# Kernel tuning notes

Measured on AMD Instinct MI355X. Metric: run time of the kernel, lower is better.

The kernel has to match this reference:

```python
import jax, jax.numpy as jnp
import numpy as np

NUM_FEATURES = 256
NUM_PIDS = 5554          # must equal hardcoded FocalLoss ignore_index
NUM_CQ = 50000
N_ROIS = 2048
OIM_SCALAR = 30.0
IGNORE_INDEX = 5554
ALPHA = 1.0
GAMMA = 2.0


def _l2norm(x):
    return x / jnp.linalg.norm(x, axis=-1, keepdims=True)


def setup_inputs() -> dict:
    key = jax.random.key(0)
    k1, k2, k3, k4, k5 = jax.random.split(key, 5)
    inputs = _l2norm(jax.random.normal(k1, (N_ROIS, NUM_FEATURES), jnp.float32))
    # targets >= 1 so label = targets-1 >= 0 (the inds filter is all-True -> static shapes)
    # targets == NUM_PIDS+1 -> label == NUM_PIDS == ignore_index (unlabeled, ignored in loss)
    targets = jax.random.randint(k2, (N_ROIS,), 1, NUM_PIDS + 2, dtype=jnp.int64)
    ious = jax.random.uniform(k3, (N_ROIS,), jnp.float32)
    lut = _l2norm(jax.random.normal(k4, (NUM_PIDS, NUM_FEATURES), jnp.float32))
    cq = _l2norm(jax.random.normal(k5, (NUM_CQ, NUM_FEATURES), jnp.float32))
    return {"inputs": inputs, "lut": lut, "cq": cq, "targets": targets, "ious": ious}


def _focal_loss(logits, labels):
    # F.cross_entropy(reduction='none', ignore_index=IGNORE_INDEX) then
    # focal = alpha * (1-pt)^gamma * ce, mean over ALL samples (ignored -> 0).
    logp = jax.nn.log_softmax(logits, axis=-1)                       # [N, C]
    ce = -jnp.take_along_axis(logp, labels[:, None], axis=1)[:, 0]   # [N]
    ce = jnp.where(labels == IGNORE_INDEX, 0.0, ce)
    pt = jnp.exp(-ce)
    return jnp.mean(ALPHA * (1.0 - pt) ** GAMMA * ce)


def reference(inputs, lut, cq, targets, ious):
    # targets = cat(roi_label); label = targets - 1; inds all True by construction.
    label = targets - 1
    # LOIM forward: logits against labeled LUT and unlabeled circular queue.
    table = jnp.concatenate([lut, cq], axis=0)          # [P+Q, D]
    projected = OIM_SCALAR * (inputs @ table.T)         # [N, P+Q]
    loss_oim = _focal_loss(projected, label)
    return loss_oim, inputs, label
```

## Files before the change

### kernel.cpp

```cpp
#include <hip/hip_runtime.h>
#include <hip/hip_bf16.h>


#define NFEAT 256
#define NROIS 2048
#define NPIDS 5554
#define NCLS 55554
#define NCHUNKS 3473
#define NCLSP 55584
#define S2F 43.280851226668906f
#define LN2F 0.6931471805599453f
#define LOFF 524289

typedef float f32x4 __attribute__((ext_vector_type(4)));
typedef short bf16x8 __attribute__((ext_vector_type(8)));
typedef unsigned short u16x8 __attribute__((ext_vector_type(8)));

#if __has_builtin(__builtin_amdgcn_exp2f)
#define EXP2(x) __builtin_amdgcn_exp2f(x)
#else
#define EXP2(x) exp2f(x)
#endif

__device__ __forceinline__ short bfb(float x) {
    return __builtin_bit_cast(short, __float2bfloat16(x));
}

__device__ __forceinline__ void gll16(const void* g, void* l) {
    __builtin_amdgcn_global_load_lds(
        (const __attribute__((address_space(1))) void*)g,
        (__attribute__((address_space(3))) void*)l, 16, 0, 0);
}

__global__ __launch_bounds__(256) void preprocess(
        const float* __restrict__ inputs, const float* __restrict__ lut,
        const float* __restrict__ cq, const int* __restrict__ cand0,
        const int* __restrict__ cand1, unsigned short* __restrict__ tb,
        unsigned short* __restrict__ ab, int* __restrict__ lab,
        float* __restrict__ S, float* __restrict__ f, const int useTB) {
    const int tid = threadIdx.x;
    const int bx = blockIdx.x;

    if (bx == 0) {
        __shared__ int smode;
        __shared__ const int* sT;
        if (tid == 0) {
            const int* T = cand0;
            const unsigned u0 = (unsigned)cand0[0];
            const float f0 = __builtin_bit_cast(float, cand0[0]);
            const bool oki = (u0 >= 1u && u0 <= 6000u);
            const bool okf = (f0 >= 1.0f && f0 <= 6000.0f);
            if (!oki && !okf) T = cand1;
            int mode = 0;
            const unsigned tu0 = (unsigned)T[0];
            const float tf0 = __builtin_bit_cast(float, T[0]);
            if (tu0 >= 1u && tu0 <= 6000u) mode = ((T[1] | T[3] | T[5] | T[7]) == 0) ? 1 : 0;
            else if (tf0 >= 1.0f && tf0 <= 6000.0f) mode = 2;
            smode = mode; sT = T;
        }
        __syncthreads();
        const int mode = smode;
        const int* T = sT;
        for (int j = tid; j < NROIS; j += 256) {
            int tv;
            if (mode == 1)      tv = T[2 * j];
            else if (mode == 2) tv = (int)__builtin_bit_cast(float, T[j]);
            else                tv = T[j];
            const int lv = tv - 1;
            lab[j] = lv;
            f[LOFF + j] = __bfloat162float(__float2bfloat16((float)lv));
        }
        for (int j = tid; j < NROIS + 8; j += 256) S[j] = 0.0f;
    }

    if (bx < 512) {
        const int i = bx * 256 + tid;
        const float4 v = *reinterpret_cast<const float4*>(inputs + (size_t)i * 4);
        float* o = f + 1 + (size_t)i * 4;
        o[0] = v.x; o[1] = v.y; o[2] = v.z; o[3] = v.w;
        if (useTB) {
            ushort4 u;
            u.x = (unsigned short)bfb(v.x); u.y = (unsigned short)bfb(v.y);
            u.z = (unsigned short)bfb(v.z); u.w = (unsigned short)bfb(v.w);
            *reinterpret_cast<ushort4*>(ab + (size_t)i * 4) = u;
        }
    }

    if (useTB) {
        const size_t LUTN = (size_t)NPIDS * NFEAT;
        const size_t TOT  = (size_t)NCLS * NFEAT;
        const size_t TOTP = (size_t)NCLSP * NFEAT;
        const size_t stride = (size_t)gridDim.x * 256 * 8;
        for (size_t e = ((size_t)bx * 256 + tid) * 8; e < TOTP; e += stride) {
            u16x8 o = {0, 0, 0, 0, 0, 0, 0, 0};
            if (e < TOT) {
                const float* sp = (e < LUTN) ? (lut + e) : (cq + (e - LUTN));
                const float4 a = *reinterpret_cast<const float4*>(sp);
                const float4 b = *reinterpret_cast<const float4*>(sp + 4);
                o[0] = (unsigned short)bfb(a.x); o[1] = (unsigned short)bfb(a.y);
                o[2] = (unsigned short)bfb(a.z); o[3] = (unsigned short)bfb(a.w);
                o[4] = (unsigned short)bfb(b.x); o[5] = (unsigned short)bfb(b.y);
                o[6] = (unsigned short)bfb(b.z); o[7] = (unsigned short)bfb(b.w);
            }
            *reinterpret_cast<u16x8*>(tb + e) = o;
        }
    }
}

template <bool TB>
__global__ __launch_bounds__(256, 2) void main_gemm8(const float* __restrict__ inputs,
                                                     const unsigned short* __restrict__ tb,
                                                     const unsigned short* __restrict__ ab,
                                                     const float* __restrict__ lut,
                                                     const float* __restrict__ cq,
                                                     float* __restrict__ S) {
    __shared__ char lds[65536];
    const int tid = threadIdx.x;
    const int lane = tid & 63;
    const int wave = tid >> 6;
    const int cs = blockIdx.x & 63;
    const int rg = blockIdx.x >> 6;
    const int rowbase = rg * 256 + wave * 64;
    const int li = lane & 15;
    const int q = lane >> 4;
    const int xorli = 4 * (li & 7);
    char* const lbase = &lds[0];

    float sums[4][4] = {{0.f,0.f,0.f,0.f},{0.f,0.f,0.f,0.f},
                        {0.f,0.f,0.f,0.f},{0.f,0.f,0.f,0.f}};

    if constexpr (TB) {
        bf16x8 afrag[4][8];
        #pragma unroll
        for (int s = 0; s < 4; s++) {
            const unsigned short* rp = ab + (size_t)(rowbase + s * 16 + li) * NFEAT + q * 8;
            #pragma unroll
            for (int kc = 0; kc < 8; kc++)
                afrag[s][kc] = *reinterpret_cast<const bf16x8*>(rp + kc * 32);
        }
        asm volatile("s_waitcnt vmcnt(0)" ::: "memory");

        const int hi = lane >> 5;
        const int lo = lane & 31;
        const int u0 = lo ^ (4 * hi);
        char* const wb = lbase + wave * 16384;

        const int cA = (cs * NCHUNKS) >> 6;
        const int cB = ((cs + 1) * NCHUNKS) >> 6;
        const int NB = cB - cA;

        #define STAGE(c16, buf)                                                     \
            {                                                                        \
                _Pragma("unroll")                                                    \
                for (int g = 0; g < 8; g++) {                                        \
                    const unsigned short* src = tb +                                 \
                        (size_t)((c16) * 16 + 2 * g + hi) * NFEAT +                  \
                        (u0 ^ (8 * (g & 3))) * 8;                                    \
                    gll16(src, wb + (buf) * 8192 + g * 1024);                        \
                }                                                                    \
            }

        STAGE(cA, 0);
        for (int i = 0; i < NB; ++i) {
            if (i + 1 < NB) {
                STAGE(cA + i + 1, (i + 1) & 1);
                asm volatile("s_waitcnt vmcnt(8)" ::: "memory");
            } else {
                asm volatile("s_waitcnt vmcnt(0)" ::: "memory");
            }
            char* const cbuf = wb + (i & 1) * 8192;
            bf16x8 bfr[8];
            #pragma unroll
            for (int kc = 0; kc < 8; kc++) {
                const int slot = li * 32 + ((q + 4 * kc) ^ xorli);
                bfr[kc] = *reinterpret_cast<const bf16x8*>(cbuf + slot * 16);
            }
            f32x4 acc[4] = {{0.f,0.f,0.f,0.f},{0.f,0.f,0.f,0.f},
                            {0.f,0.f,0.f,0.f},{0.f,0.f,0.f,0.f}};
            __builtin_amdgcn_s_setprio(1);
            #pragma unroll
            for (int kc = 0; kc < 8; kc++) {
                acc[0] = __builtin_amdgcn_mfma_f32_16x16x32_bf16(afrag[0][kc], bfr[kc], acc[0], 0, 0, 0);
                acc[1] = __builtin_amdgcn_mfma_f32_16x16x32_bf16(afrag[1][kc], bfr[kc], acc[1], 0, 0, 0);
                acc[2] = __builtin_amdgcn_mfma_f32_16x16x32_bf16(afrag[2][kc], bfr[kc], acc[2], 0, 0, 0);
                acc[3] = __builtin_amdgcn_mfma_f32_16x16x32_bf16(afrag[3][kc], bfr[kc], acc[3], 0, 0, 0);
            }
            __builtin_amdgcn_s_setprio(0);
            #pragma unroll
            for (int s = 0; s < 4; s++)
                #pragma unroll
                for (int r = 0; r < 4; r++)
                    sums[s][r] += EXP2(S2F * acc[s][r] - S2F);
        }
        #undef STAGE
    } else {
        bf16x8 afrag[4][8];
        #pragma unroll
        for (int s = 0; s < 4; s++) {
            const float* rp = inputs + (size_t)(rowbase + s * 16 + li) * NFEAT + q * 8;
            #pragma unroll
            for (int kc = 0; kc < 8; kc++) {
                const float4 x0 = *reinterpret_cast<const float4*>(rp + kc * 32);
                const float4 x1 = *reinterpret_cast<const float4*>(rp + kc * 32 + 4);
                bf16x8 a;
                a[0] = bfb(x0.x); a[1] = bfb(x0.y); a[2] = bfb(x0.z); a[3] = bfb(x0.w);
                a[4] = bfb(x1.x); a[5] = bfb(x1.y); a[6] = bfb(x1.z); a[7] = bfb(x1.w);
                afrag[s][kc] = a;
            }
        }
        short* fb = (short*)lbase;
        const int s0 = tid, s1 = tid + 256;
        const int cc0 = s0 >> 5, cc1 = s1 >> 5;
        const int uo0 = ((s0 & 31) ^ (4 * (cc0 & 7))) * 8;
        const int uo1 = ((s1 & 31) ^ (4 * (cc1 & 7))) * 8;
        const int cA = (cs * NCHUNKS) >> 6;
        const int cB = ((cs + 1) * NCHUNKS) >> 6;
        {
            int n0 = cA * 16 + cc0; n0 = n0 < (NCLS - 1) ? n0 : (NCLS - 1);
            int n1 = cA * 16 + cc1; n1 = n1 < (NCLS - 1) ? n1 : (NCLS - 1);
            const float* r0 = ((n0 < NPIDS) ? lut + (size_t)n0 * NFEAT
                                            : cq + (size_t)(n0 - NPIDS) * NFEAT) + uo0;
            const float* r1 = ((n1 < NPIDS) ? lut + (size_t)n1 * NFEAT
                                            : cq + (size_t)(n1 - NPIDS) * NFEAT) + uo1;
            const float4 a0 = *reinterpret_cast<const float4*>(r0);
            const float4 a1 = *reinterpret_cast<const float4*>(r0 + 4);
            const float4 b0 = *reinterpret_cast<const float4*>(r1);
            const float4 b1 = *reinterpret_cast<const float4*>(r1 + 4);
            bf16x8 v0, v1;
            v0[0]=bfb(a0.x); v0[1]=bfb(a0.y); v0[2]=bfb(a0.z); v0[3]=bfb(a0.w);
            v0[4]=bfb(a1.x); v0[5]=bfb(a1.y); v0[6]=bfb(a1.z); v0[7]=bfb(a1.w);
            v1[0]=bfb(b0.x); v1[1]=bfb(b0.y); v1[2]=bfb(b0.z); v1[3]=bfb(b0.w);
            v1[4]=bfb(b1.x); v1[5]=bfb(b1.y); v1[6]=bfb(b1.z); v1[7]=bfb(b1.w);
            *reinterpret_cast<bf16x8*>(&fb[s0 * 8]) = v0;
            *reinterpret_cast<bf16x8*>(&fb[s1 * 8]) = v1;
        }
        __syncthreads();
        int cur = 0;
        for (int ci = cA; ci < cB; ++ci) {
            const bool pf = (ci + 1 < cB);
            float4 f0a, f0b, f1a, f1b;
            if (pf) {
                int n0 = (ci + 1) * 16 + cc0; n0 = n0 < (NCLS - 1) ? n0 : (NCLS - 1);
                int n1 = (ci + 1) * 16 + cc1; n1 = n1 < (NCLS - 1) ? n1 : (NCLS - 1);
                const float* r0 = ((n0 < NPIDS) ? lut + (size_t)n0 * NFEAT
                                                : cq + (size_t)(n0 - NPIDS) * NFEAT) + uo0;
                const float* r1 = ((n1 < NPIDS) ? lut + (size_t)n1 * NFEAT
                                                : cq + (size_t)(n1 - NPIDS) * NFEAT) + uo1;
                f0a = *reinterpret_cast<const float4*>(r0);
                f0b = *reinterpret_cast<const float4*>(r0 + 4);
                f1a = *reinterpret_cast<const float4*>(r1);
                f1b = *reinterpret_cast<const float4*>(r1 + 4);
            }
            f32x4 acc[4] = {{0.f,0.f,0.f,0.f},{0.f,0.f,0.f,0.f},
                            {0.f,0.f,0.f,0.f},{0.f,0.f,0.f,0.f}};
            #pragma unroll
            for (int kc = 0; kc < 8; kc++) {
                const int slot = li * 32 + ((q + 4 * kc) ^ xorli);
                const bf16x8 b = *reinterpret_cast<const bf16x8*>(&fb[cur * 4096 + slot * 8]);
                acc[0] = __builtin_amdgcn_mfma_f32_16x16x32_bf16(afrag[0][kc], b, acc[0], 0, 0, 0);
                acc[1] = __builtin_amdgcn_mfma_f32_16x16x32_bf16(afrag[1][kc], b, acc[1], 0, 0, 0);
                acc[2] = __builtin_amdgcn_mfma_f32_16x16x32_bf16(afrag[2][kc], b, acc[2], 0, 0, 0);
                acc[3] = __builtin_amdgcn_mfma_f32_16x16x32_bf16(afrag[3][kc], b, acc[3], 0, 0, 0);
            }
            const float valid = ((ci * 16 + li) < NCLS) ? 1.0f : 0.0f;
            #pragma unroll
            for (int s = 0; s < 4; s++)
                #pragma unroll
                for (int r = 0; r < 4; r++)
                    sums[s][r] += valid * EXP2(S2F * (acc[s][r] - 1.0f));
            if (pf) {
                bf16x8 p0, p1;
                p0[0]=bfb(f0a.x); p0[1]=bfb(f0a.y); p0[2]=bfb(f0a.z); p0[3]=bfb(f0a.w);
                p0[4]=bfb(f0b.x); p0[5]=bfb(f0b.y); p0[6]=bfb(f0b.z); p0[7]=bfb(f0b.w);
                p1[0]=bfb(f1a.x); p1[1]=bfb(f1a.y); p1[2]=bfb(f1a.z); p1[3]=bfb(f1a.w);
                p1[4]=bfb(f1b.x); p1[5]=bfb(f1b.y); p1[6]=bfb(f1b.z); p1[7]=bfb(f1b.w);
                *reinterpret_cast<bf16x8*>(&fb[(cur ^ 1) * 4096 + s0 * 8]) = p0;
                *reinterpret_cast<bf16x8*>(&fb[(cur ^ 1) * 4096 + s1 * 8]) = p1;
            }
            __syncthreads();
            cur ^= 1;
        }
    }

    #pragma unroll
    for (int s = 0; s < 4; s++)
        #pragma unroll
        for (int r = 0; r < 4; r++) {
            float v = sums[s][r];
            v += __shfl_xor(v, 1); v += __shfl_xor(v, 2);
            v += __shfl_xor(v, 4); v += __shfl_xor(v, 8);
            sums[s][r] = v;
        }
    if (li == 0) {
        #pragma unroll
        for (int s = 0; s < 4; s++)
            #pragma unroll
            for (int r = 0; r < 4; r++)
                atomicAdd(&S[rowbase + s * 16 + q * 4 + r], sums[s][r]);
    }
}

__global__ __launch_bounds__(256) void focal_final(const float* __restrict__ inputs,
                                                   const float* __restrict__ lut,
                                                   const int* __restrict__ lab,
                                                   const float* __restrict__ S,
                                                   float* __restrict__ loss_acc,
                                                   unsigned int* __restrict__ cnt,
                                                   float* __restrict__ f) {
    const int wave = threadIdx.x >> 6;
    const int lane = threadIdx.x & 63;
    const int row = blockIdx.x * 4 + wave;
    const int label = lab[row];
    const bool valid = (label >= 0 && label < NPIDS);
    const int lr = valid ? label : 0;
    const float4 a = *reinterpret_cast<const float4*>(inputs + (size_t)row * NFEAT + lane * 4);
    const float4 b = *reinterpret_cast<const float4*>(lut + (size_t)lr * NFEAT + lane * 4);
    float v = a.x * b.x + a.y * b.y + a.z * b.z + a.w * b.w;
    #pragma unroll
    for (int m = 1; m < 64; m <<= 1) v += __shfl_xor(v, m);

    __shared__ float red[4];
    if (lane == 0) {
        float fo = 0.0f;
        if (valid) {
            const float l2 = v * S2F;
            const float lse2 = S2F + log2f(S[row]);
            float ce = fmaxf((lse2 - l2) * LN2F, 0.0f);
            const float pt = EXP2(l2 - lse2);
            const float om = 1.0f - pt;
            fo = om * om * ce;
        }
        red[wave] = fo;
    }
    __syncthreads();
    if (threadIdx.x == 0) {
        atomicAdd(loss_acc, red[0] + red[1] + red[2] + red[3]);
        __threadfence();
        const unsigned done = atomicAdd(cnt, 1u) + 1u;
        if (done == gridDim.x) {
            const float tot = atomicAdd(loss_acc, 0.0f);
            f[0] = tot * (1.0f / NROIS);
        }
    }
}

extern "C" void kernel_launch(void* const* d_in, const int* in_sizes, int n_in,
                              void* d_out, int out_size, void* d_ws, size_t ws_size,
                              hipStream_t stream) {
    const float* inputs = (const float*)d_in[0];
    const float* lut    = (const float*)d_in[1];
    const float* cq     = (const float*)d_in[2];
    const int*   cand0  = (const int*)d_in[3];
    const int*   cand1  = (const int*)((n_in > 4) ? d_in[4] : d_in[3]);
    float* f = (float*)d_out;

    const size_t TBB = (size_t)NCLSP * NFEAT * 2;
    const size_t ABB = (size_t)NROIS * NFEAT * 2;
    char* ws = (char*)d_ws;
    const bool useTB = ws_size >= TBB + ABB + 32768;

    unsigned short* tb = useTB ? (unsigned short*)ws : nullptr;
    unsigned short* ab = useTB ? (unsigned short*)(ws + TBB) : nullptr;
    float* S = useTB ? (float*)(ws + TBB + ABB) : (float*)ws;
    float* loss_acc    = S + NROIS;
    unsigned int* cnt  = (unsigned int*)(S + NROIS + 1);
    int* lab           = (int*)(S + NROIS + 8);

    preprocess<<<useTB ? 4096 : 512, 256, 0, stream>>>(inputs, lut, cq, cand0, cand1,
                                                       tb, ab, lab, S, f, useTB ? 1 : 0);
    if (useTB) main_gemm8<true><<<512, 256, 0, stream>>>(inputs, tb, ab, lut, cq, S);
    else       main_gemm8<false><<<512, 256, 0, stream>>>(inputs, tb, ab, lut, cq, S);
    focal_final<<<512, 256, 0, stream>>>(inputs, lut, lab, S, loss_acc, cnt, f);
}
```

Measured before the change: 176.4 us.

## Share 48-column table tiles across waves with triple-buffered block-wide staging

```diff
diff --git a/kernel.cpp b/kernel.cpp
--- a/kernel.cpp
+++ b/kernel.cpp
@@ -7,7 +7,8 @@
 #define NPIDS 5554
 #define NCLS 55554
 #define NCHUNKS 3473
-#define NCLSP 55584
+#define NCH48 1158
+#define NCLSP (NCH48 * 48)
 #define S2F 43.280851226668906f
 #define LN2F 0.6931471805599453f
 #define LOFF 524289
@@ -108,13 +109,13 @@
 }
 
 template <bool TB>
-__global__ __launch_bounds__(256, 2) void main_gemm8(const float* __restrict__ inputs,
-                                                     const unsigned short* __restrict__ tb,
-                                                     const unsigned short* __restrict__ ab,
-                                                     const float* __restrict__ lut,
-                                                     const float* __restrict__ cq,
-                                                     float* __restrict__ S) {
-    __shared__ char lds[65536];
+__global__ __launch_bounds__(256, 2) void main_gemm10(const float* __restrict__ inputs,
+                                                      const unsigned short* __restrict__ tb,
+                                                      const unsigned short* __restrict__ ab,
+                                                      const float* __restrict__ lut,
+                                                      const float* __restrict__ cq,
+                                                      float* __restrict__ S) {
+    __shared__ char lds[73728];
     const int tid = threadIdx.x;
     const int lane = tid & 63;
     const int wave = tid >> 6;
@@ -140,57 +141,57 @@
         }
         asm volatile("s_waitcnt vmcnt(0)" ::: "memory");
 
-        const int hi = lane >> 5;
-        const int lo = lane & 31;
-        const int u0 = lo ^ (4 * hi);
-        char* const wb = lbase + wave * 16384;
-
-        const int cA = (cs * NCHUNKS) >> 6;
-        const int cB = ((cs + 1) * NCHUNKS) >> 6;
+        const int cc0 = tid >> 5;
+        const int uo = ((tid & 31) ^ (4 * cc0)) * 8;
+        const int ldd = wave * 1024;
+        const int cA = (cs * NCH48) >> 6;
+        const int cB = ((cs + 1) * NCH48) >> 6;
         const int NB = cB - cA;
-
-        #define STAGE(c16, buf)                                                     \
+        const unsigned short* psrc = tb + (size_t)(cA * 48 + cc0) * NFEAT + uo;
+        int ob0 = 0, ob1 = 24576, ob2 = 49152;
+
+        #define STAGE(ob)                                                            \
             {                                                                        \
                 _Pragma("unroll")                                                    \
-                for (int g = 0; g < 8; g++) {                                        \
-                    const unsigned short* src = tb +                                 \
-                        (size_t)((c16) * 16 + 2 * g + hi) * NFEAT +                  \
-                        (u0 ^ (8 * (g & 3))) * 8;                                    \
-                    gll16(src, wb + (buf) * 8192 + g * 1024);                        \
-                }                                                                    \
-            }
-
-        STAGE(cA, 0);
+                for (int k = 0; k < 6; k++)                                          \
+                    gll16(psrc + (size_t)(8 * k) * NFEAT, lbase + (ob) + ldd + k * 4096); \
+                psrc += (size_t)48 * NFEAT;                                          \
+            }
+
+        STAGE(ob0);
+        if (NB > 1) STAGE(ob1);
+
         for (int i = 0; i < NB; ++i) {
-            if (i + 1 < NB) {
-                STAGE(cA + i + 1, (i + 1) & 1);
-                asm volatile("s_waitcnt vmcnt(8)" ::: "memory");
-            } else {
-                asm volatile("s_waitcnt vmcnt(0)" ::: "memory");
-            }
-            char* const cbuf = wb + (i & 1) * 8192;
-            bf16x8 bfr[8];
-            #pragma unroll
-            for (int kc = 0; kc < 8; kc++) {
-                const int slot = li * 32 + ((q + 4 * kc) ^ xorli);
-                bfr[kc] = *reinterpret_cast<const bf16x8*>(cbuf + slot * 16);
-            }
-            f32x4 acc[4] = {{0.f,0.f,0.f,0.f},{0.f,0.f,0.f,0.f},
-                            {0.f,0.f,0.f,0.f},{0.f,0.f,0.f,0.f}};
-            __builtin_amdgcn_s_setprio(1);
-            #pragma unroll
-            for (int kc = 0; kc < 8; kc++) {
-                acc[0] = __builtin_amdgcn_mfma_f32_16x16x32_bf16(afrag[0][kc], bfr[kc], acc[0], 0, 0, 0);
-                acc[1] = __builtin_amdgcn_mfma_f32_16x16x32_bf16(afrag[1][kc], bfr[kc], acc[1], 0, 0, 0);
-                acc[2] = __builtin_amdgcn_mfma_f32_16x16x32_bf16(afrag[2][kc], bfr[kc], acc[2], 0, 0, 0);
-                acc[3] = __builtin_amdgcn_mfma_f32_16x16x32_bf16(afrag[3][kc], bfr[kc], acc[3], 0, 0, 0);
-            }
-            __builtin_amdgcn_s_setprio(0);
-            #pragma unroll
-            for (int s = 0; s < 4; s++)
+            if (i + 1 < NB) asm volatile("s_waitcnt vmcnt(6)\n\ts_barrier" ::: "memory");
+            else            asm volatile("s_waitcnt vmcnt(0)\n\ts_barrier" ::: "memory");
+            if (i + 2 < NB) STAGE(ob2);
+            #pragma unroll
+            for (int h = 0; h < 3; h++) {
+                const int cc = h * 16 + li;
+                bf16x8 bfr[8];
                 #pragma unroll
-                for (int r = 0; r < 4; r++)
-                    sums[s][r] += EXP2(S2F * acc[s][r] - S2F);
+                for (int kc = 0; kc < 8; kc++) {
+                    const int slot = cc * 32 + ((q + 4 * kc) ^ xorli);
+                    bfr[kc] = *reinterpret_cast<const bf16x8*>(lbase + ob0 + slot * 16);
+                }
+                f32x4 acc[4] = {{0.f,0.f,0.f,0.f},{0.f,0.f,0.f,0.f},
+                                {0.f,0.f,0.f,0.f},{0.f,0.f,0.f,0.f}};
+                __builtin_amdgcn_s_setprio(1);
+                #pragma unroll
+                for (int kc = 0; kc < 8; kc++) {
+                    acc[0] = __builtin_amdgcn_mfma_f32_16x16x32_bf16(afrag[0][kc], bfr[kc], acc[0], 0, 0, 0);
+                    acc[1] = __builtin_amdgcn_mfma_f32_16x16x32_bf16(afrag[1][kc], bfr[kc], acc[1], 0, 0, 0);
+                    acc[2] = __builtin_amdgcn_mfma_f32_16x16x32_bf16(afrag[2][kc], bfr[kc], acc[2], 0, 0, 0);
+                    acc[3] = __builtin_amdgcn_mfma_f32_16x16x32_bf16(afrag[3][kc], bfr[kc], acc[3], 0, 0, 0);
+                }
+                __builtin_amdgcn_s_setprio(0);
+                #pragma unroll
+                for (int s = 0; s < 4; s++)
+                    #pragma unroll
+                    for (int r = 0; r < 4; r++)
+                        sums[s][r] += EXP2(S2F * acc[s][r] - S2F);
+            }
+            const int t = ob0; ob0 = ob1; ob1 = ob2; ob2 = t;
         }
         #undef STAGE
     } else {
@@ -368,7 +369,7 @@
 
     preprocess<<<useTB ? 4096 : 512, 256, 0, stream>>>(inputs, lut, cq, cand0, cand1,
                                                        tb, ab, lab, S, f, useTB ? 1 : 0);
-    if (useTB) main_gemm8<true><<<512, 256, 0, stream>>>(inputs, tb, ab, lut, cq, S);
-    else       main_gemm8<false><<<512, 256, 0, stream>>>(inputs, tb, ab, lut, cq, S);
+    if (useTB) main_gemm10<true><<<512, 256, 0, stream>>>(inputs, tb, ab, lut, cq, S);
+    else       main_gemm10<false><<<512, 256, 0, stream>>>(inputs, tb, ab, lut, cq, S);
     focal_final<<<512, 256, 0, stream>>>(inputs, lut, lab, S, loss_acc, cnt, f);
 }
```

Measured after the change: 175.3 us. Within noise of the previous version (-0.6%).
